# Kernel optimization log

Hardware: AMD Instinct MI355X
Metric: run time of the kernel (lower is better)

Reference implementation:

```python
import jax, jax.numpy as jnp
import numpy as np

N = 50000      # nodes
E = 800000     # edges (avg degree 16)
D = 128        # feature / channel width (channel_counts=[128,128,128])
HEAD = 64      # head_dim
NEG_SLOPE = 0.2  # PyG GATConv leaky_relu slope


def setup_inputs() -> dict:
    key = jax.random.key(0)
    ks = jax.random.split(key, 32)
    s = 1.0 / np.sqrt(D)

    def w(k, shape):
        return jax.random.normal(k, shape, jnp.float32) * s

    return {
        "x": jax.random.normal(ks[0], (N, D), jnp.float32),
        "edge_index": jax.random.randint(ks[1], (2, E), 0, N, dtype=jnp.int32),
        # layer 0: lazy (-1,-1) GATConv -> separate src/dst linear maps
        "w0_src": w(ks[2], (D, D)), "w0_dst": w(ks[3], (D, D)),
        "a0_src": w(ks[4], (D,)), "a0_dst": w(ks[5], (D,)),
        "bc0": jnp.zeros((D,), jnp.float32),
        "wl0": w(ks[6], (D, D)), "bl0": jnp.zeros((D,), jnp.float32),
        # layer 1: int in_channels -> shared weight
        "w1": w(ks[7], (D, D)),
        "a1_src": w(ks[8], (D,)), "a1_dst": w(ks[9], (D,)),
        "bc1": jnp.zeros((D,), jnp.float32),
        "wl1": w(ks[10], (D, D)), "bl1": jnp.zeros((D,), jnp.float32),
        # layer 2
        "w2": w(ks[11], (D, D)),
        "a2_src": w(ks[12], (D,)), "a2_dst": w(ks[13], (D,)),
        "bc2": jnp.zeros((D,), jnp.float32),
        "wl2": w(ks[14], (D, D)), "bl2": jnp.zeros((D,), jnp.float32),
        # head linear
        "wh": w(ks[15], (D, HEAD)), "bh": jnp.zeros((HEAD,), jnp.float32),
    }


def _gat(h_src, h_dst, src, dst, a_src, a_dst, bias):
    """PyG GATConv (heads=1, no self loops, eval-mode). h_*: [N,C]."""
    al_s = h_src @ a_src                                   # [N]
    al_d = h_dst @ a_dst                                   # [N]
    logits = jax.nn.leaky_relu(al_s[src] + al_d[dst], NEG_SLOPE)  # [E]
    m = jax.ops.segment_max(logits, dst, num_segments=N)  # per-dest max
    e = jnp.exp(logits - m[dst])
    denom = jax.ops.segment_sum(e, dst, num_segments=N)
    alpha = e / denom[dst]                                 # [E]
    msg = h_src[src] * alpha[:, None]                      # [E,C]
    return jax.ops.segment_sum(msg, dst, num_segments=N) + bias


def reference(x, edge_index, w0_src, w0_dst, a0_src, a0_dst, bc0, wl0, bl0,
              w1, a1_src, a1_dst, bc1, wl1, bl1,
              w2, a2_src, a2_dst, bc2, wl2, bl2, wh, bh):
    src, dst = edge_index[0], edge_index[1]
    # layer 0: conv(x) + lin(x), relu
    h = _gat(x @ w0_src, x @ w0_dst, src, dst, a0_src, a0_dst, bc0) + x @ wl0 + bl0
    h = jax.nn.relu(h)
    # layer 1: shared-weight conv
    hs = h @ w1
    h = _gat(hs, hs, src, dst, a1_src, a1_dst, bc1) + h @ wl1 + bl1
    h = jax.nn.relu(h)
    # layer 2 (no relu)
    hs = h @ w2
    h = _gat(hs, hs, src, dst, a2_src, a2_dst, bc2) + h @ wl2 + bl2
    # head
    return h @ wh + bh
```

## Files before the change

### kernel.cpp

```cpp
#include <hip/hip_runtime.h>

#define NNODE 50000
#define NEDGE 800000
#define DIM   128
#define NEG   0.2f
#define NBUCK 196
#define EPB1  2048
#define NB1   391
#define GBLK  782
#define GN    12500
#define SB_PA (NB1)
#define SB_PH (SB_PA + 32)
#define SB_MV (SB_PH + 65)
#define SB_CV (SB_MV + 193)
#define SB_TOT (SB_CV + GN)
#define SCX   (NBUCK + 1 + GN)

typedef __attribute__((ext_vector_type(8))) short bf16x8;
typedef __attribute__((ext_vector_type(4))) float f32x4;

__device__ __forceinline__ float wmax(float v){
  #pragma unroll
  for (int m = 32; m > 0; m >>= 1) v = fmaxf(v, __shfl_xor(v, m));
  return v;
}
__device__ __forceinline__ float wsum(float v){
  #pragma unroll
  for (int m = 32; m > 0; m >>= 1) v += __shfl_xor(v, m);
  return v;
}
__device__ __forceinline__ unsigned short f2bf(float f){
  unsigned int x = __float_as_uint(f);
  return (unsigned short)((x + 0x7fffu + ((x >> 16) & 1u)) >> 16);
}
__device__ __forceinline__ float bflo(unsigned u){ return __uint_as_float(u << 16); }
__device__ __forceinline__ float bfhi(unsigned u){ return __uint_as_float(u & 0xffff0000u); }

__global__ __launch_bounds__(256) void setup_k(
    const int* __restrict__ ei,
    const float* __restrict__ x,
    const float* __restrict__ w0s, const float* __restrict__ a0s,
    const float* __restrict__ w0d, const float* __restrict__ a0d,
    const float* __restrict__ bc0, const float* __restrict__ wl0,
    const float* __restrict__ bl0,
    const float* __restrict__ w1,  const float* __restrict__ a1s,
    const float* __restrict__ a1d, const float* __restrict__ bc1,
    const float* __restrict__ wl1, const float* __restrict__ bl1,
    const float* __restrict__ w2,  const float* __restrict__ a2s,
    const float* __restrict__ a2d, const float* __restrict__ bc2,
    const float* __restrict__ wl2, const float* __restrict__ bl2,
    const float* __restrict__ wh,  const float* __restrict__ bh,
    int* __restrict__ cnt,
    unsigned short* __restrict__ Wz1, unsigned short* __restrict__ Wz2,
    unsigned short* __restrict__ Wz3, float* __restrict__ bf3,
    float* __restrict__ uv, float* __restrict__ bf1, float* __restrict__ bf2,
    unsigned int* __restrict__ Xb){
  int bid = blockIdx.x;

  if (bid < NB1){
    __shared__ int h[NBUCK];
    const int* dst = ei + NEDGE;
    for (int i = threadIdx.x; i < NBUCK; i += 256) h[i] = 0;
    __syncthreads();
    int e0 = bid * EPB1 + threadIdx.x;
    #pragma unroll
    for (int i = 0; i < 8; ++i){
      int e = e0 + i * 256;
      if (e < NEDGE) atomicAdd(&h[dst[e] >> 8], 1);
    }
    __syncthreads();
    for (int i = threadIdx.x; i < NBUCK; i += 256)
      cnt[i * NB1 + bid] = h[i];
    return;
  }
  if (bid < SB_PH){
    int g = (bid - SB_PA) * 256 + threadIdx.x;
    int layer = g >> 12;
    int rem = g & 4095;
    int ct = rem >> 9, q = (rem >> 6) & 7, lane = rem & 63;
    int quad = lane >> 4;
    int c = ct * 16 + (lane & 15);
    const float* wA = layer ? w1 : w0s;
    const float* wB = layer ? wl1 : wl0;
    unsigned short* dst = (layer ? Wz2 : Wz1) + ((size_t)(ct * 8 + q) * 64 + lane) * 8;
    #pragma unroll
    for (int j = 0; j < 8; ++j){
      int k = q * 32 + quad * 8 + j;
      float v = (k < 128) ? wA[k * 128 + c] : wB[(k - 128) * 128 + c];
      dst[j] = f2bf(v);
    }
    return;
  }
  if (bid < SB_MV){
    int pb = bid - SB_PH;
    if (pb == 64){
      int c = threadIdx.x;
      if (c < 64){
        float s = bh[c];
        for (int t = 0; t < 128; ++t) s += (bc2[t] + bl2[t]) * wh[t * 64 + c];
        bf3[c] = s;
      }
      return;
    }
    int g = pb * 256 + threadIdx.x;
    int k = g >> 6, c = g & 63;
    const float* src = (k < 128) ? (w2 + k * 128) : (wl2 + (k - 128) * 128);
    float s = 0.f;
    for (int t = 0; t < 128; ++t) s += src[t] * wh[t * 64 + c];
    int ct = c >> 4, q = k >> 5, quad = (k >> 3) & 3, j = k & 7;
    int ln = quad * 16 + (c & 15);
    Wz3[((size_t)(ct * 8 + q) * 64 + ln) * 8 + j] = f2bf(s);
    return;
  }
  if (bid < SB_CV){
    int mb = bid - SB_MV;
    if (mb == 192){
      int t = threadIdx.x;
      if (t < 128) bf1[t] = bc0[t] + bl0[t];
      else bf2[t - 128] = bc1[t - 128] + bl1[t - 128];
      return;
    }
    int lane = threadIdx.x & 63;
    int idx = mb * 4 + (threadIdx.x >> 6);
    int grp = idx >> 7, r = idx & 127;
    const float* W; const float* a;
    switch (grp){
      case 0: W = w0s; a = a0s; break;
      case 1: W = w0d; a = a0d; break;
      case 2: W = w1;  a = a1s; break;
      case 3: W = w1;  a = a1d; break;
      case 4: W = w2;  a = a2s; break;
      default: W = w2; a = a2d; break;
    }
    float2 w = ((const float2*)(W + r * DIM))[lane];
    float2 av = ((const float2*)a)[lane];
    float s = wsum(w.x * av.x + w.y * av.y);
    if (lane == 0) uv[grp * 128 + r] = s;
    return;
  }
  {
    int lane = threadIdx.x & 63;
    int n = (bid - SB_CV) * 4 + (threadIdx.x >> 6);
    if (n >= NNODE) return;
    float2 xv = ((const float2*)(x + (size_t)n * DIM))[lane];
    Xb[(size_t)n * 64 + lane] = (unsigned)f2bf(xv.x) | ((unsigned)f2bf(xv.y) << 16);
  }
}

__global__ __launch_bounds__(256) void scanx_k(const int* __restrict__ cnt,
                                               int* __restrict__ cbase,
                                               int* __restrict__ gbase,
                                               int* __restrict__ rp,
                                               const float* __restrict__ X,
                                               const float* __restrict__ uv,
                                               float* __restrict__ als,
                                               float* __restrict__ ald){
  int bid = blockIdx.x, t = threadIdx.x;
  if (bid < NBUCK){
    __shared__ int sd[256];
    const int* row = cnt + (size_t)bid * NB1;
    int i0 = t * 2, i1 = t * 2 + 1;
    int v0 = (i0 < NB1) ? row[i0] : 0;
    int v1 = (i1 < NB1) ? row[i1] : 0;
    int s = v0 + v1;
    sd[t] = s; __syncthreads();
    #pragma unroll
    for (int off = 1; off < 256; off <<= 1){
      int u = (t >= off) ? sd[t - off] : 0;
      __syncthreads();
      sd[t] += u;
      __syncthreads();
    }
    int ex = sd[t] - s;
    if (i0 < NB1) cbase[(size_t)bid * NB1 + i0] = ex;
    if (i1 < NB1) cbase[(size_t)bid * NB1 + i1] = ex + v0;
    return;
  }
  if (bid == NBUCK){
    __shared__ int sd[256];
    int tot = 0;
    if (t < NBUCK){
      const int* row = cnt + (size_t)t * NB1;
      for (int j = 0; j < NB1; ++j) tot += row[j];
    }
    sd[t] = tot; __syncthreads();
    #pragma unroll
    for (int off = 1; off < 256; off <<= 1){
      int u = (t >= off) ? sd[t - off] : 0;
      __syncthreads();
      sd[t] += u;
      __syncthreads();
    }
    if (t < NBUCK) gbase[t] = sd[t] - tot;
    if (t == NBUCK - 1) gbase[NBUCK] = sd[t];
    if (t == 0) rp[NNODE] = NEDGE;
    return;
  }
  {
    int lane = t & 63;
    int n = (bid - NBUCK - 1) * 4 + (t >> 6);
    if (n >= NNODE) return;
    float2 xv = ((const float2*)(X + (size_t)n * DIM))[lane];
    float2 uu = ((const float2*)uv)[lane];
    float2 vv = ((const float2*)(uv + 128))[lane];
    float s1 = wsum(xv.x * uu.x + xv.y * uu.y);
    float s2 = wsum(xv.x * vv.x + xv.y * vv.y);
    if (lane == 0){ als[n] = s1; ald[n] = s2; }
  }
}

__global__ __launch_bounds__(256) void scat2_k(const int* __restrict__ ei,
                                               const int* __restrict__ gbase,
                                               const int* __restrict__ cbase,
                                               unsigned int* __restrict__ packed){
  __shared__ int lcur[NBUCK];
  for (int i = threadIdx.x; i < NBUCK; i += 256) lcur[i] = 0;
  __syncthreads();
  int e0 = blockIdx.x * EPB1 + threadIdx.x;
  #pragma unroll
  for (int i = 0; i < 8; ++i){
    int e = e0 + i * 256;
    if (e < NEDGE){
      int s = ei[e], d = ei[NEDGE + e];
      int b = d >> 8;
      int r = atomicAdd(&lcur[b], 1);
      int pos = gbase[b] + cbase[(size_t)b * NB1 + blockIdx.x] + r;
      packed[pos] = ((unsigned)d << 16) | (unsigned)s;
    }
  }
}

__global__ __launch_bounds__(256) void build_k(const int* __restrict__ gbase,
                                               const unsigned int* __restrict__ packed,
                                               int* __restrict__ rp,
                                               unsigned short* __restrict__ es){
  __shared__ int h[256], sd[256], cur[256];
  int b = blockIdx.x, t = threadIdx.x;
  int s0 = gbase[b], s1 = gbase[b + 1];
  h[t] = 0; __syncthreads();
  for (int i = s0 + t; i < s1; i += 256)
    atomicAdd(&h[(packed[i] >> 16) & 255], 1);
  __syncthreads();
  int v = h[t]; sd[t] = v; __syncthreads();
  #pragma unroll
  for (int off = 1; off < 256; off <<= 1){
    int u = (t >= off) ? sd[t - off] : 0;
    __syncthreads();
    sd[t] += u;
    __syncthreads();
  }
  int ex = sd[t] - v;
  cur[t] = ex;
  int d = b * 256 + t;
  if (d < NNODE) rp[d] = s0 + ex;
  __syncthreads();
  for (int i = s0 + t; i < s1; i += 256){
    unsigned int p = packed[i];
    int ld = (p >> 16) & 255;
    int pos = atomicAdd(&cur[ld], 1);
    es[s0 + pos] = (unsigned short)(p & 0xffffu);
  }
}

__global__ __launch_bounds__(256) void gat_k(const int* __restrict__ rp,
                                             const unsigned short* __restrict__ es,
                                             const float* __restrict__ als,
                                             const float* __restrict__ ald,
                                             const unsigned int* __restrict__ A,
                                             unsigned int* __restrict__ Mb){
  int lane = threadIdx.x & 63;
  int n = blockIdx.x * 4 + (threadIdx.x >> 6);
  if (n >= NNODE) return;
  int start = rp[n], end = rp[n + 1];
  int deg = end - start;
  float ad = ald[n];
  int half = lane >> 4, sub = lane & 15;
  const uint4* A4 = (const uint4*)A;

  if (deg <= 32){
    int s = (lane < deg) ? (int)es[start + lane] : 0;

    int s0 = __shfl(s, half),      s1 = __shfl(s, 4 + half);
    int s2 = __shfl(s, 8 + half),  s3 = __shfl(s, 12 + half);
    uint4 p0 = A4[(size_t)s0 * 16 + sub];
    uint4 p1 = A4[(size_t)s1 * 16 + sub];
    uint4 p2 = A4[(size_t)s2 * 16 + sub];
    uint4 p3 = A4[(size_t)s3 * 16 + sub];
    uint4 p4, p5, p6, p7;
    bool big = deg > 16;
    if (big){
      int s4 = __shfl(s, 16 + half), s5 = __shfl(s, 20 + half);
      int s6 = __shfl(s, 24 + half), s7 = __shfl(s, 28 + half);
      p4 = A4[(size_t)s4 * 16 + sub];
      p5 = A4[(size_t)s5 * 16 + sub];
      p6 = A4[(size_t)s6 * 16 + sub];
      p7 = A4[(size_t)s7 * 16 + sub];
    }

    float z = -3.0e38f;
    if (lane < deg){
      float t = als[s] + ad;
      z = t > 0.f ? t : NEG * t;
    }
    float m = wmax(z);
    float e = (lane < deg) ? __expf(z - m) : 0.f;
    float denom = wsum(e);
    float rinv = (deg > 0) ? 1.f / denom : 0.f;

    float w0 = __shfl(e, half),      w1 = __shfl(e, 4 + half);
    float w2 = __shfl(e, 8 + half),  w3 = __shfl(e, 12 + half);
    float a0=0.f,a1=0.f,a2=0.f,a3=0.f,a4=0.f,a5=0.f,a6=0.f,a7=0.f;
    a0 = fmaf(w0, bflo(p0.x), a0); a1 = fmaf(w0, bfhi(p0.x), a1);
    a2 = fmaf(w0, bflo(p0.y), a2); a3 = fmaf(w0, bfhi(p0.y), a3);
    a4 = fmaf(w0, bflo(p0.z), a4); a5 = fmaf(w0, bfhi(p0.z), a5);
    a6 = fmaf(w0, bflo(p0.w), a6); a7 = fmaf(w0, bfhi(p0.w), a7);
    a0 = fmaf(w1, bflo(p1.x), a0); a1 = fmaf(w1, bfhi(p1.x), a1);
    a2 = fmaf(w1, bflo(p1.y), a2); a3 = fmaf(w1, bfhi(p1.y), a3);
    a4 = fmaf(w1, bflo(p1.z), a4); a5 = fmaf(w1, bfhi(p1.z), a5);
    a6 = fmaf(w1, bflo(p1.w), a6); a7 = fmaf(w1, bfhi(p1.w), a7);
    a0 = fmaf(w2, bflo(p2.x), a0); a1 = fmaf(w2, bfhi(p2.x), a1);
    a2 = fmaf(w2, bflo(p2.y), a2); a3 = fmaf(w2, bfhi(p2.y), a3);
    a4 = fmaf(w2, bflo(p2.z), a4); a5 = fmaf(w2, bfhi(p2.z), a5);
    a6 = fmaf(w2, bflo(p2.w), a6); a7 = fmaf(w2, bfhi(p2.w), a7);
    a0 = fmaf(w3, bflo(p3.x), a0); a1 = fmaf(w3, bfhi(p3.x), a1);
    a2 = fmaf(w3, bflo(p3.y), a2); a3 = fmaf(w3, bfhi(p3.y), a3);
    a4 = fmaf(w3, bflo(p3.z), a4); a5 = fmaf(w3, bfhi(p3.z), a5);
    a6 = fmaf(w3, bflo(p3.w), a6); a7 = fmaf(w3, bfhi(p3.w), a7);
    if (big){
      float w4 = __shfl(e, 16 + half), w5 = __shfl(e, 20 + half);
      float w6 = __shfl(e, 24 + half), w7 = __shfl(e, 28 + half);
      a0 = fmaf(w4, bflo(p4.x), a0); a1 = fmaf(w4, bfhi(p4.x), a1);
      a2 = fmaf(w4, bflo(p4.y), a2); a3 = fmaf(w4, bfhi(p4.y), a3);
      a4 = fmaf(w4, bflo(p4.z), a4); a5 = fmaf(w4, bfhi(p4.z), a5);
      a6 = fmaf(w4, bflo(p4.w), a6); a7 = fmaf(w4, bfhi(p4.w), a7);
      a0 = fmaf(w5, bflo(p5.x), a0); a1 = fmaf(w5, bfhi(p5.x), a1);
      a2 = fmaf(w5, bflo(p5.y), a2); a3 = fmaf(w5, bfhi(p5.y), a3);
      a4 = fmaf(w5, bflo(p5.z), a4); a5 = fmaf(w5, bfhi(p5.z), a5);
      a6 = fmaf(w5, bflo(p5.w), a6); a7 = fmaf(w5, bfhi(p5.w), a7);
      a0 = fmaf(w6, bflo(p6.x), a0); a1 = fmaf(w6, bfhi(p6.x), a1);
      a2 = fmaf(w6, bflo(p6.y), a2); a3 = fmaf(w6, bfhi(p6.y), a3);
      a4 = fmaf(w6, bflo(p6.z), a4); a5 = fmaf(w6, bfhi(p6.z), a5);
      a6 = fmaf(w6, bflo(p6.w), a6); a7 = fmaf(w6, bfhi(p6.w), a7);
      a0 = fmaf(w7, bflo(p7.x), a0); a1 = fmaf(w7, bfhi(p7.x), a1);
      a2 = fmaf(w7, bflo(p7.y), a2); a3 = fmaf(w7, bfhi(p7.y), a3);
      a4 = fmaf(w7, bflo(p7.z), a4); a5 = fmaf(w7, bfhi(p7.z), a5);
      a6 = fmaf(w7, bflo(p7.w), a6); a7 = fmaf(w7, bfhi(p7.w), a7);
    }
    #define RED(vv) vv += __shfl_xor(vv, 16); vv += __shfl_xor(vv, 32);
    RED(a0) RED(a1) RED(a2) RED(a3) RED(a4) RED(a5) RED(a6) RED(a7)
    #undef RED
    if (half == 0){
      uint4 o;
      o.x = (unsigned)f2bf(a0 * rinv) | ((unsigned)f2bf(a1 * rinv) << 16);
      o.y = (unsigned)f2bf(a2 * rinv) | ((unsigned)f2bf(a3 * rinv) << 16);
      o.z = (unsigned)f2bf(a4 * rinv) | ((unsigned)f2bf(a5 * rinv) << 16);
      o.w = (unsigned)f2bf(a6 * rinv) | ((unsigned)f2bf(a7 * rinv) << 16);
      ((uint4*)(Mb + (size_t)n * 64))[sub] = o;
    }
    return;
  }

  if (deg <= 64){
    int s = 0; float z = -3.0e38f;
    if (lane < deg){
      s = es[start + lane];
      float t = als[s] + ad;
      z = t > 0.f ? t : NEG * t;
    }
    float m = wmax(z);
    float e = (lane < deg) ? __expf(z - m) : 0.f;
    float denom = wsum(e);
    float rinv = (deg > 0) ? 1.f / denom : 0.f;

    float a0=0.f,a1=0.f,a2=0.f,a3=0.f,a4=0.f,a5=0.f,a6=0.f,a7=0.f;
    int dq = (deg + 7) & ~7;
    for (int j = 0; j < dq; j += 8){
      int   sA = __shfl(s, j + half);
      int   sB = __shfl(s, j + 4 + half);
      float wA = __shfl(e, j + half);
      float wB = __shfl(e, j + 4 + half);
      uint4 pA = A4[(size_t)sA * 16 + sub];
      uint4 pB = A4[(size_t)sB * 16 + sub];
      a0 = fmaf(wA, bflo(pA.x), a0); a1 = fmaf(wA, bfhi(pA.x), a1);
      a2 = fmaf(wA, bflo(pA.y), a2); a3 = fmaf(wA, bfhi(pA.y), a3);
      a4 = fmaf(wA, bflo(pA.z), a4); a5 = fmaf(wA, bfhi(pA.z), a5);
      a6 = fmaf(wA, bflo(pA.w), a6); a7 = fmaf(wA, bfhi(pA.w), a7);
      a0 = fmaf(wB, bflo(pB.x), a0); a1 = fmaf(wB, bfhi(pB.x), a1);
      a2 = fmaf(wB, bflo(pB.y), a2); a3 = fmaf(wB, bfhi(pB.y), a3);
      a4 = fmaf(wB, bflo(pB.z), a4); a5 = fmaf(wB, bfhi(pB.z), a5);
      a6 = fmaf(wB, bflo(pB.w), a6); a7 = fmaf(wB, bfhi(pB.w), a7);
    }
    #define RED(vv) vv += __shfl_xor(vv, 16); vv += __shfl_xor(vv, 32);
    RED(a0) RED(a1) RED(a2) RED(a3) RED(a4) RED(a5) RED(a6) RED(a7)
    #undef RED
    if (half == 0){
      uint4 o;
      o.x = (unsigned)f2bf(a0 * rinv) | ((unsigned)f2bf(a1 * rinv) << 16);
      o.y = (unsigned)f2bf(a2 * rinv) | ((unsigned)f2bf(a3 * rinv) << 16);
      o.z = (unsigned)f2bf(a4 * rinv) | ((unsigned)f2bf(a5 * rinv) << 16);
      o.w = (unsigned)f2bf(a6 * rinv) | ((unsigned)f2bf(a7 * rinv) << 16);
      ((uint4*)(Mb + (size_t)n * 64))[sub] = o;
    }
  } else {
    float2 acc = make_float2(0.f, 0.f);
    float mloc = -3.0e38f;
    for (int i = start + lane; i < end; i += 64){
      int s = es[i];
      float zz = als[s] + ad;
      zz = zz > 0.f ? zz : NEG * zz;
      mloc = fmaxf(mloc, zz);
    }
    float m = wmax(mloc);
    float dloc = 0.f;
    for (int i = start + lane; i < end; i += 64){
      int s = es[i];
      float zz = als[s] + ad;
      zz = zz > 0.f ? zz : NEG * zz;
      dloc += __expf(zz - m);
    }
    float rinv = 1.f / wsum(dloc);
    for (int i = start; i < end; ++i){
      int s = es[i];
      float zz = als[s] + ad;
      zz = zz > 0.f ? zz : NEG * zz;
      float w = __expf(zz - m);
      unsigned p = A[(size_t)s * 64 + lane];
      acc.x = fmaf(w, bflo(p), acc.x);
      acc.y = fmaf(w, bfhi(p), acc.y);
    }
    Mb[(size_t)n * 64 + lane] =
        (unsigned)f2bf(acc.x * rinv) | ((unsigned)f2bf(acc.y * rinv) << 16);
  }
}

template<int FINAL>
__global__ __launch_bounds__(256) void mfma_k(const unsigned int* __restrict__ Mb,
                                              const unsigned int* __restrict__ Hin,
                                              const unsigned short* __restrict__ Wz,
                                              const float* __restrict__ bias,
                                              const float* __restrict__ u,
                                              const float* __restrict__ v,
                                              unsigned short* __restrict__ Hout,
                                              float* __restrict__ outf,
                                              float* __restrict__ als,
                                              float* __restrict__ ald){
  int lane = threadIdx.x & 63;
  int wid  = threadIdx.x >> 6;
  int r0   = blockIdx.x * 64 + wid * 16;
  int quad = lane >> 4;
  int col  = lane & 15;

  int rA = r0 + col; if (rA > NNODE - 1) rA = NNODE - 1;
  const bf16x8* mrow = (const bf16x8*)(Mb + (size_t)rA * 64);
  const bf16x8* hrow = (const bf16x8*)(Hin + (size_t)rA * 64);
  bf16x8 a[8];
  #pragma unroll
  for (int q = 0; q < 4; ++q){
    a[q]     = mrow[q * 4 + quad];
    a[q + 4] = hrow[q * 4 + quad];
  }

  const bf16x8* wz = (const bf16x8*)Wz;
  int rowq = r0 + quad * 4;
  float alsp[4] = {0.f, 0.f, 0.f, 0.f};
  float aldp[4] = {0.f, 0.f, 0.f, 0.f};
  const int NCT = FINAL ? 4 : 8;

  #pragma unroll
  for (int ct = 0; ct < NCT; ++ct){
    if (!FINAL && ct == 4) __syncthreads();
    f32x4 acc = {0.f, 0.f, 0.f, 0.f};
    #pragma unroll
    for (int q = 0; q < 8; ++q){
      bf16x8 bfr = wz[(ct * 8 + q) * 64 + lane];
      acc = __builtin_amdgcn_mfma_f32_16x16x32_bf16(a[q], bfr, acc, 0, 0, 0);
    }
    int c = ct * 16 + col;
    float bb = bias[c];
    if (FINAL){
      #pragma unroll
      for (int r = 0; r < 4; ++r){
        int row = rowq + r;
        if (row < NNODE) outf[(size_t)row * 64 + c] = acc[r] + bb;
      }
    } else {
      float uc = u[c], vc = v[c];
      #pragma unroll
      for (int r = 0; r < 4; ++r){
        float h = fmaxf(acc[r] + bb, 0.f);
        alsp[r] = fmaf(h, uc, alsp[r]);
        aldp[r] = fmaf(h, vc, aldp[r]);
        int row = rowq + r;
        if (row < NNODE) Hout[(size_t)row * 128 + c] = f2bf(h);
      }
    }
  }

  if (!FINAL){
    #pragma unroll
    for (int m = 1; m < 16; m <<= 1){
      #pragma unroll
      for (int r = 0; r < 4; ++r){
        alsp[r] += __shfl_xor(alsp[r], m);
        aldp[r] += __shfl_xor(aldp[r], m);
      }
    }
    if (col == 0){
      #pragma unroll
      for (int r = 0; r < 4; ++r){
        int row = rowq + r;
        if (row < NNODE){ als[row] = alsp[r]; ald[row] = aldp[r]; }
      }
    }
  }
}

extern "C" void kernel_launch(void* const* d_in, const int* in_sizes, int n_in,
                              void* d_out, int out_size, void* d_ws, size_t ws_size,
                              hipStream_t stream){
  const float* x   = (const float*)d_in[0];
  const int*   ei  = (const int*)d_in[1];
  const float* w0s = (const float*)d_in[2];
  const float* w0d = (const float*)d_in[3];
  const float* a0s = (const float*)d_in[4];
  const float* a0d = (const float*)d_in[5];
  const float* bc0 = (const float*)d_in[6];
  const float* wl0 = (const float*)d_in[7];
  const float* bl0 = (const float*)d_in[8];
  const float* w1  = (const float*)d_in[9];
  const float* a1s = (const float*)d_in[10];
  const float* a1d = (const float*)d_in[11];
  const float* bc1 = (const float*)d_in[12];
  const float* wl1 = (const float*)d_in[13];
  const float* bl1 = (const float*)d_in[14];
  const float* w2  = (const float*)d_in[15];
  const float* a2s = (const float*)d_in[16];
  const float* a2d = (const float*)d_in[17];
  const float* bc2 = (const float*)d_in[18];
  const float* wl2 = (const float*)d_in[19];
  const float* bl2 = (const float*)d_in[20];
  const float* wh  = (const float*)d_in[21];
  const float* bh  = (const float*)d_in[22];
  float* out = (float*)d_out;

  unsigned int* Xb = (unsigned int*)d_ws;
  unsigned int* Ha = Xb + (size_t)NNODE * 64;
  unsigned int* Hb = Ha + (size_t)NNODE * 64;
  unsigned int* Mb = Hb + (size_t)NNODE * 64;
  float* alsA = (float*)(Mb + (size_t)NNODE * 64);
  float* aldA = alsA + NNODE;
  float* alsB = aldA + NNODE;
  float* aldB = alsB + NNODE;
  float* uv   = aldB + NNODE;
  float* bf1  = uv + 6 * 128;
  float* bf2  = bf1 + 128;
  float* bf3  = bf2 + 128;
  unsigned short* Wz1 = (unsigned short*)(bf3 + 64);
  unsigned short* Wz2 = Wz1 + 256 * 128;
  unsigned short* Wz3 = Wz2 + 256 * 128;
  int*   rp    = (int*)(Wz3 + 256 * 64);
  int*   cnt   = rp + (NNODE + 1);
  int*   cbase = cnt + NBUCK * NB1;
  int*   btot  = cbase + NBUCK * NB1;
  int*   gbase = btot + NBUCK;
  unsigned int* packed = (unsigned int*)(gbase + (NBUCK + 1));
  unsigned short* es   = (unsigned short*)(packed + NEDGE);

  dim3 b(256);
  dim3 gn(GN);

  setup_k<<<SB_TOT, b, 0, stream>>>(ei, x,
      w0s, a0s, w0d, a0d, bc0, wl0, bl0,
      w1, a1s, a1d, bc1, wl1, bl1,
      w2, a2s, a2d, bc2, wl2, bl2, wh, bh,
      cnt, Wz1, Wz2, Wz3, bf3, uv, bf1, bf2, Xb);

  scanx_k<<<SCX, b, 0, stream>>>(cnt, cbase, gbase, rp, x, uv, alsA, aldA);
  scat2_k<<<NB1, b, 0, stream>>>(ei, gbase, cbase, packed);
  build_k<<<NBUCK, b, 0, stream>>>(gbase, packed, rp, es);

  gat_k<<<gn, b, 0, stream>>>(rp, es, alsA, aldA, Xb, Mb);
  mfma_k<0><<<GBLK, b, 0, stream>>>(Mb, Xb, Wz1, bf1, uv + 2 * 128, uv + 3 * 128,
                                    (unsigned short*)Ha, nullptr, alsB, aldB);

  gat_k<<<gn, b, 0, stream>>>(rp, es, alsB, aldB, Ha, Mb);
  mfma_k<0><<<GBLK, b, 0, stream>>>(Mb, Ha, Wz2, bf2, uv + 4 * 128, uv + 5 * 128,
                                    (unsigned short*)Hb, nullptr, alsA, aldA);

  gat_k<<<gn, b, 0, stream>>>(rp, es, alsA, aldA, Hb, Mb);
  mfma_k<1><<<GBLK, b, 0, stream>>>(Mb, Hb, Wz3, bf3, nullptr, nullptr,
                                    nullptr, out, nullptr, nullptr);
}
```

Before: 281.1 us.

## Parallelize bucket totals, widen build and MFMA blocks, hoist als load

The bucket-total pass in scanx_k now has each wavefront sum one bucket row with a warp reduction, replacing the serial per-thread loop over 391 counts. build_k and mfma_k are launched with 512 threads, and mfma_k covers 128 rows per block with half as many blocks. In gat_k the als[s] gather is issued early, alongside the feature loads, so its latency overlaps with them. Larger blocks may lower occupancy or change scheduling in the MFMA kernel, and mfma_k's shared-memory use at the new block size is not visible here.

```diff
diff --git a/kernel.cpp b/kernel.cpp
--- a/kernel.cpp
+++ b/kernel.cpp
@@ -7,7 +7,7 @@
 #define NBUCK 196
 #define EPB1  2048
 #define NB1   391
-#define GBLK  782
+#define GBLK  391
 #define GN    12500
 #define SB_PA (NB1)
 #define SB_PH (SB_PA + 32)
@@ -25,6 +25,11 @@
   return v;
 }
 __device__ __forceinline__ float wsum(float v){
+  #pragma unroll
+  for (int m = 32; m > 0; m >>= 1) v += __shfl_xor(v, m);
+  return v;
+}
+__device__ __forceinline__ int wsumi(int v){
   #pragma unroll
   for (int m = 32; m > 0; m >>= 1) v += __shfl_xor(v, m);
   return v;
@@ -177,13 +182,19 @@
     return;
   }
   if (bid == NBUCK){
+    __shared__ int bt[NBUCK];
     __shared__ int sd[256];
-    int tot = 0;
-    if (t < NBUCK){
-      const int* row = cnt + (size_t)t * NB1;
-      for (int j = 0; j < NB1; ++j) tot += row[j];
-    }
-    sd[t] = tot; __syncthreads();
+    int w = t >> 6, lane = t & 63;
+    for (int bkt = w; bkt < NBUCK; bkt += 4){
+      const int* row = cnt + (size_t)bkt * NB1;
+      int sum = 0;
+      for (int j = lane; j < NB1; j += 64) sum += row[j];
+      sum = wsumi(sum);
+      if (lane == 0) bt[bkt] = sum;
+    }
+    __syncthreads();
+    int v = (t < NBUCK) ? bt[t] : 0;
+    sd[t] = v; __syncthreads();
     #pragma unroll
     for (int off = 1; off < 256; off <<= 1){
       int u = (t >= off) ? sd[t - off] : 0;
@@ -191,7 +202,7 @@
       sd[t] += u;
       __syncthreads();
     }
-    if (t < NBUCK) gbase[t] = sd[t] - tot;
+    if (t < NBUCK) gbase[t] = sd[t] - v;
     if (t == NBUCK - 1) gbase[NBUCK] = sd[t];
     if (t == 0) rp[NNODE] = NEDGE;
     return;
@@ -230,31 +241,36 @@
   }
 }
 
-__global__ __launch_bounds__(256) void build_k(const int* __restrict__ gbase,
+__global__ __launch_bounds__(512) void build_k(const int* __restrict__ gbase,
                                                const unsigned int* __restrict__ packed,
                                                int* __restrict__ rp,
                                                unsigned short* __restrict__ es){
   __shared__ int h[256], sd[256], cur[256];
   int b = blockIdx.x, t = threadIdx.x;
   int s0 = gbase[b], s1 = gbase[b + 1];
-  h[t] = 0; __syncthreads();
-  for (int i = s0 + t; i < s1; i += 256)
+  if (t < 256) h[t] = 0;
+  __syncthreads();
+  for (int i = s0 + t; i < s1; i += 512)
     atomicAdd(&h[(packed[i] >> 16) & 255], 1);
   __syncthreads();
-  int v = h[t]; sd[t] = v; __syncthreads();
+  int v = (t < 256) ? h[t] : 0;
+  if (t < 256) sd[t] = v;
+  __syncthreads();
   #pragma unroll
   for (int off = 1; off < 256; off <<= 1){
-    int u = (t >= off) ? sd[t - off] : 0;
+    int u = (t >= off && t < 256) ? sd[t - off] : 0;
     __syncthreads();
-    sd[t] += u;
+    if (t < 256) sd[t] += u;
     __syncthreads();
   }
-  int ex = sd[t] - v;
-  cur[t] = ex;
-  int d = b * 256 + t;
-  if (d < NNODE) rp[d] = s0 + ex;
+  if (t < 256){
+    int ex = sd[t] - v;
+    cur[t] = ex;
+    int d = b * 256 + t;
+    if (d < NNODE) rp[d] = s0 + ex;
+  }
   __syncthreads();
-  for (int i = s0 + t; i < s1; i += 256){
+  for (int i = s0 + t; i < s1; i += 512){
     unsigned int p = packed[i];
     int ld = (p >> 16) & 255;
     int pos = atomicAdd(&cur[ld], 1);
@@ -279,6 +295,7 @@
 
   if (deg <= 32){
     int s = (lane < deg) ? (int)es[start + lane] : 0;
+    float alv = (lane < deg) ? als[s] : 0.f;
 
     int s0 = __shfl(s, half),      s1 = __shfl(s, 4 + half);
     int s2 = __shfl(s, 8 + half),  s3 = __shfl(s, 12 + half);
@@ -299,7 +316,7 @@
 
     float z = -3.0e38f;
     if (lane < deg){
-      float t = als[s] + ad;
+      float t = alv + ad;
       z = t > 0.f ? t : NEG * t;
     }
     float m = wmax(z);
@@ -434,7 +451,7 @@
 }
 
 template<int FINAL>
-__global__ __launch_bounds__(256) void mfma_k(const unsigned int* __restrict__ Mb,
+__global__ __launch_bounds__(512) void mfma_k(const unsigned int* __restrict__ Mb,
                                               const unsigned int* __restrict__ Hin,
                                               const unsigned short* __restrict__ Wz,
                                               const float* __restrict__ bias,
@@ -446,7 +463,7 @@
                                               float* __restrict__ ald){
   int lane = threadIdx.x & 63;
   int wid  = threadIdx.x >> 6;
-  int r0   = blockIdx.x * 64 + wid * 16;
+  int r0   = blockIdx.x * 128 + wid * 16;
   int quad = lane >> 4;
   int col  = lane & 15;
 
@@ -567,6 +584,7 @@
   unsigned short* es   = (unsigned short*)(packed + NEDGE);
 
   dim3 b(256);
+  dim3 b2(512);
   dim3 gn(GN);
 
   setup_k<<<SB_TOT, b, 0, stream>>>(ei, x,
@@ -577,17 +595,17 @@
 
   scanx_k<<<SCX, b, 0, stream>>>(cnt, cbase, gbase, rp, x, uv, alsA, aldA);
   scat2_k<<<NB1, b, 0, stream>>>(ei, gbase, cbase, packed);
-  build_k<<<NBUCK, b, 0, stream>>>(gbase, packed, rp, es);
+  build_k<<<NBUCK, b2, 0, stream>>>(gbase, packed, rp, es);
 
   gat_k<<<gn, b, 0, stream>>>(rp, es, alsA, aldA, Xb, Mb);
-  mfma_k<0><<<GBLK, b, 0, stream>>>(Mb, Xb, Wz1, bf1, uv + 2 * 128, uv + 3 * 128,
-                                    (unsigned short*)Ha, nullptr, alsB, aldB);
+  mfma_k<0><<<GBLK, b2, 0, stream>>>(Mb, Xb, Wz1, bf1, uv + 2 * 128, uv + 3 * 128,
+                                     (unsigned short*)Ha, nullptr, alsB, aldB);
 
   gat_k<<<gn, b, 0, stream>>>(rp, es, alsB, aldB, Ha, Mb);
-  mfma_k<0><<<GBLK, b, 0, stream>>>(Mb, Ha, Wz2, bf2, uv + 4 * 128, uv + 5 * 128,
-                                    (unsigned short*)Hb, nullptr, alsA, aldA);
+  mfma_k<0><<<GBLK, b2, 0, stream>>>(Mb, Ha, Wz2, bf2, uv + 4 * 128, uv + 5 * 128,
+                                     (unsigned short*)Hb, nullptr, alsA, aldA);
 
   gat_k<<<gn, b, 0, stream>>>(rp, es, alsA, aldA, Hb, Mb);
-  mfma_k<1><<<GBLK, b, 0, stream>>>(Mb, Hb, Wz3, bf3, nullptr, nullptr,
-                                    nullptr, out, nullptr, nullptr);
-}
+  mfma_k<1><<<GBLK, b2, 0, stream>>>(Mb, Hb, Wz3, bf3, nullptr, nullptr,
+                                     nullptr, out, nullptr, nullptr);
+}
```

After: 360.7 us. 1.28x slower.
